# Optimization experiments

Measured on AMD Instinct MI355X. Metric: run time of the kernel, lower is better.

The kernel has to match this reference:

```python
import jax, jax.numpy as jnp
import numpy as np

D_MODEL = 512
NHEAD = 8
DK = D_MODEL // NHEAD
DIM_FF = 2048
LN_EPS = 1e-5


def setup_inputs() -> dict:
    key = jax.random.key(0)
    ks = jax.random.split(key, 12)
    B, L = 8, 1024
    s = 1.0 / np.sqrt(D_MODEL)
    sf = 1.0 / np.sqrt(DIM_FF)
    return {
        "x": jax.random.normal(ks[0], (B, L, D_MODEL), jnp.float32),
        "key_padding_mask": jnp.zeros((B, L), dtype=bool),
        "bias": jax.random.normal(ks[1], (B, L, L), jnp.float32),
        # projection weights stored [in, out] so y = x @ W + b (matches torch Linear math)
        "Wq": jax.random.normal(ks[2], (D_MODEL, D_MODEL), jnp.float32) * s,
        "bq": jnp.zeros((D_MODEL,), jnp.float32),
        "Wk": jax.random.normal(ks[3], (D_MODEL, D_MODEL), jnp.float32) * s,
        "bk": jnp.zeros((D_MODEL,), jnp.float32),
        "Wv": jax.random.normal(ks[4], (D_MODEL, D_MODEL), jnp.float32) * s,
        "bv": jnp.zeros((D_MODEL,), jnp.float32),
        "Wo": jax.random.normal(ks[5], (D_MODEL, D_MODEL), jnp.float32) * s,
        "bo": jnp.zeros((D_MODEL,), jnp.float32),
        "ln1_g": jnp.ones((D_MODEL,), jnp.float32),
        "ln1_b": jnp.zeros((D_MODEL,), jnp.float32),
        "W1": jax.random.normal(ks[6], (D_MODEL, DIM_FF), jnp.float32) * s,
        "b1": jnp.zeros((DIM_FF,), jnp.float32),
        "W2": jax.random.normal(ks[7], (DIM_FF, D_MODEL), jnp.float32) * sf,
        "b2": jnp.zeros((D_MODEL,), jnp.float32),
        "ln2_g": jnp.ones((D_MODEL,), jnp.float32),
        "ln2_b": jnp.zeros((D_MODEL,), jnp.float32),
    }


def _layernorm(x, g, b):
    mu = jnp.mean(x, axis=-1, keepdims=True)
    var = jnp.mean(jnp.square(x - mu), axis=-1, keepdims=True)
    return (x - mu) * jax.lax.rsqrt(var + LN_EPS) * g + b


def reference(x, key_padding_mask, bias, Wq, bq, Wk, bk, Wv, bv, Wo, bo,
              ln1_g, ln1_b, W1, b1, W2, b2, ln2_g, ln2_b):
    B, L, H = x.shape
    residual = x
    # [B, L, D] -> [B, nhead, L, dk]
    q = (x @ Wq + bq).reshape(B, L, NHEAD, DK).transpose(0, 2, 1, 3)
    k = (x @ Wk + bk).reshape(B, L, NHEAD, DK).transpose(0, 2, 1, 3)
    v = (x @ Wv + bv).reshape(B, L, NHEAD, DK).transpose(0, 2, 1, 3)
    scores = jnp.einsum("bhqd,bhkd->bhqk", q, k) / np.sqrt(DK)
    scores = scores + bias[:, None, :, :]
    scores = jnp.where(key_padding_mask[:, None, None, :], -jnp.inf, scores)
    attn = jax.nn.softmax(scores, axis=-1)  # dropout p=0 (eval)
    out = jnp.einsum("bhqk,bhkd->bhqd", attn, v)
    out = out.transpose(0, 2, 1, 3).reshape(B, L, H)
    out = out @ Wo + bo
    x = _layernorm(residual + out, ln1_g, ln1_b)
    residual = x
    h = jax.nn.relu(x @ W1 + b1)
    x = h @ W2 + b2
    return _layernorm(residual + x, ln2_g, ln2_b)
```

## Files before the change

### kernel.cpp

```cpp
#include <hip/hip_runtime.h>
#include <math.h>

#define NHEAD 8
#define DKD 64
#define DMODEL 512
#define LSEQ 1024
#define NBL 8192

typedef __attribute__((ext_vector_type(8))) short bf8;
typedef __attribute__((ext_vector_type(4))) float f4;

__device__ inline unsigned short f2bf(float f) {
    union { float f; unsigned u; } v; v.f = f;
    unsigned r = v.u + 0x7FFFu + ((v.u >> 16) & 1u);
    return (unsigned short)(r >> 16);
}

__device__ __forceinline__ unsigned cvtpk(float lo, float hi) {
    unsigned r;
    asm("v_cvt_pk_bf16_f32 %0, %1, %2" : "=v"(r) : "v"(lo), "v"(hi));
    return r;
}

__device__ __forceinline__ void gload16(const void* g, void* l) {
    __builtin_amdgcn_global_load_lds(
        (const __attribute__((address_space(1))) unsigned int*)g,
        (__attribute__((address_space(3))) unsigned int*)l, 16, 0, 0);
}

__global__ __launch_bounds__(256) void conv_bf16(
    const float* __restrict__ in, unsigned short* __restrict__ out, int n)
{
    int i = (blockIdx.x * 256 + threadIdx.x) * 4;
    if (i >= n) return;
    float4 v = *(const float4*)(in + i);
    ushort4 o;
    o.x = f2bf(v.x); o.y = f2bf(v.y); o.z = f2bf(v.z); o.w = f2bf(v.w);
    *(ushort4*)(out + i) = o;
}

__global__ __launch_bounds__(256) void biasm_kernel(
    const float* __restrict__ bias, const unsigned char* __restrict__ mask,
    float* __restrict__ o)
{
    int i = blockIdx.x * 256 + threadIdx.x;
    int flat = i * 4;
    int b = flat >> 20;
    int k = flat & 1023;
    float4 v = ((const float4*)bias)[i];
    uchar4 mk = *(const uchar4*)(mask + b * 1024 + k);
    if (mk.x) v.x = -1e30f;
    if (mk.y) v.y = -1e30f;
    if (mk.z) v.z = -1e30f;
    if (mk.w) v.w = -1e30f;
    ((float4*)o)[i] = v;
}

__device__ __forceinline__ void do_transpose(
    const float* __restrict__ W, unsigned short* __restrict__ Wt,
    int K, int N, int bx, int by)
{
    __shared__ float tile[64][65];
    const int k0 = by * 64, n0 = bx * 64;
    const int c = threadIdx.x & 63, r0 = (threadIdx.x >> 6) * 16;
    #pragma unroll
    for (int i = 0; i < 16; ++i)
        tile[r0 + i][c] = W[(size_t)(k0 + r0 + i) * N + n0 + c];
    __syncthreads();
    #pragma unroll
    for (int i = 0; i < 16; ++i)
        Wt[(size_t)(n0 + r0 + i) * K + k0 + c] = f2bf(tile[c][r0 + i]);
}

__global__ __launch_bounds__(256) void prep_weights(
    const float* __restrict__ Wq, const float* __restrict__ Wk,
    const float* __restrict__ Wv, const float* __restrict__ Wo,
    const float* __restrict__ W1, const float* __restrict__ W2,
    const float* __restrict__ bq, const float* __restrict__ bk,
    const float* __restrict__ bv,
    unsigned short* __restrict__ Wqkv, unsigned short* __restrict__ Wot,
    unsigned short* __restrict__ W1t, unsigned short* __restrict__ W2t,
    float* __restrict__ bqkv)
{
    int j = blockIdx.x;
    if (j < 256) {
        int which = j >> 6, tt = j & 63;
        const float* src = which == 0 ? Wq : which == 1 ? Wk : which == 2 ? Wv : Wo;
        unsigned short* dst = which == 0 ? Wqkv : which == 1 ? (Wqkv + 262144)
                            : which == 2 ? (Wqkv + 524288) : Wot;
        do_transpose(src, dst, 512, 512, tt & 7, tt >> 3);
    } else if (j < 512) {
        int tt = j - 256;
        do_transpose(W1, W1t, 512, 2048, tt & 31, tt >> 5);
    } else if (j < 768) {
        int tt = j - 512;
        do_transpose(W2, W2t, 2048, 512, tt & 7, tt >> 3);
    } else {
        for (int c = threadIdx.x; c < 1536; c += 256)
            bqkv[c] = c < 512 ? bq[c] : c < 1024 ? bk[c - 512] : bv[c - 1024];
    }
}

template<int BN>
__global__ __launch_bounds__(256) void mfma_gemm(
    const unsigned short* __restrict__ A, const unsigned short* __restrict__ Bt,
    const float* __restrict__ bias, const float* __restrict__ resid,
    void* __restrict__ outp, int M, int N, int K, int relu, int outmode,
    unsigned short* __restrict__ qs, unsigned short* __restrict__ ks,
    unsigned short* __restrict__ vts)
{
    __shared__ uint4 As[1024];
    __shared__ uint4 Bs[BN * 8];
    constexpr int NB = BN / 32;

    const int t = threadIdx.x;
    const int lane = t & 63, w = t >> 6;
    const int g = lane >> 4, r15 = lane & 15;
    const int wr = w >> 1, wc = w & 1;
    const int rowBase = blockIdx.y * 128, colBase = blockIdx.x * BN;

    f4 acc[4][NB] = {};

    const int r   = t >> 3;
    const int chs = (t & 7) ^ (r & 7);
    unsigned short* Al = (unsigned short*)As + (w * 8) * 64;
    unsigned short* Bl = (unsigned short*)Bs + (w * 8) * 64;

    for (int k0 = 0; k0 < K; k0 += 64) {
        __syncthreads();
        {
            const unsigned short* Ag = A  + (size_t)(rowBase + r) * K + k0 + chs * 8;
            const unsigned short* Bg = Bt + (size_t)(colBase + r) * K + k0 + chs * 8;
            #pragma unroll
            for (int p = 0; p < 4; ++p)
                gload16(Ag + (size_t)(p * 32) * K, Al + p * 32 * 64);
            #pragma unroll
            for (int p = 0; p < BN / 32; ++p)
                gload16(Bg + (size_t)(p * 32) * K, Bl + p * 32 * 64);
        }
        __syncthreads();
        #pragma unroll
        for (int kk = 0; kk < 2; ++kk) {
            bf8 af[4], bfr[NB];
            #pragma unroll
            for (int m = 0; m < 4; ++m) {
                int ra = wr * 64 + m * 16 + r15;
                af[m] = *(const bf8*)&As[ra * 8 + ((kk * 4 + g) ^ (ra & 7))];
            }
            #pragma unroll
            for (int n = 0; n < NB; ++n) {
                int rb = wc * (BN / 2) + n * 16 + r15;
                bfr[n] = *(const bf8*)&Bs[rb * 8 + ((kk * 4 + g) ^ (rb & 7))];
            }
            #pragma unroll
            for (int m = 0; m < 4; ++m)
                #pragma unroll
                for (int n = 0; n < NB; ++n)
                    acc[m][n] = __builtin_amdgcn_mfma_f32_16x16x32_bf16(
                        af[m], bfr[n], acc[m][n], 0, 0, 0);
        }
    }

    #pragma unroll
    for (int m = 0; m < 4; ++m) {
        #pragma unroll
        for (int n = 0; n < NB; ++n) {
            int col = colBase + wc * (BN / 2) + n * 16 + r15;
            float bv = bias[col];
            #pragma unroll
            for (int rr = 0; rr < 4; ++rr) {
                int row = rowBase + wr * 64 + m * 16 + g * 4 + rr;
                float v = acc[m][n][rr] + bv;
                if (relu) v = fmaxf(v, 0.f);
                if (outmode == 0) {
                    size_t idx = (size_t)row * N + col;
                    if (resid) v += resid[idx];
                    ((float*)outp)[idx] = v;
                } else if (outmode == 1) {
                    ((unsigned short*)outp)[(size_t)row * N + col] = f2bf(v);
                } else {
                    int sel = col >> 9, hd = col & 511;
                    int h = hd >> 6, dk = hd & 63;
                    int b = row >> 10, l = row & 1023;
                    unsigned short bw = f2bf(v);
                    size_t bh = (size_t)(b * NHEAD + h);
                    if (sel == 0)      qs[(bh * LSEQ + l) * DKD + dk] = bw;
                    else if (sel == 1) ks[(bh * LSEQ + l) * DKD + dk] = bw;
                    else               vts[(bh * DKD + dk) * LSEQ + l] = bw;
                }
            }
        }
    }
}

__global__ __launch_bounds__(256) void attn_mfma(
    const unsigned short* __restrict__ Qg, const unsigned short* __restrict__ Kg,
    const unsigned short* __restrict__ Vtg, const float* __restrict__ biasM,
    unsigned short* __restrict__ Ob)
{
    __shared__ uint4 Ks[2][512];
    __shared__ uint4 Vs[2][512];
    __shared__ unsigned int Pb[4096];

    const int t = threadIdx.x;
    const int lane = t & 63, w = t >> 6;
    const int g = lane >> 4, r15 = lane & 15;

    const int p = blockIdx.x;
    const int logical = (p & 7) * 64 + (p >> 3);
    const int bh = logical >> 3, qt = logical & 7;
    const int b = bh >> 3, h = bh & 7;
    const int qbase = qt * 128 + w * 32;

    bf8 qf[2][2];
    #pragma unroll
    for (int u = 0; u < 2; ++u) {
        const unsigned short* qp = Qg + ((size_t)bh * LSEQ + qbase + u * 16 + r15) * DKD + g * 8;
        qf[u][0] = *(const bf8*)qp;
        qf[u][1] = *(const bf8*)(qp + 32);
    }

    float mrun[2] = {-1e30f, -1e30f}, lsum[2] = {0.f, 0.f};
    f4 oacc[2][4] = {};

    const int sr  = t >> 3;
    const int chs = (t & 7) ^ (sr & 7);
    unsigned int* Pw = Pb + w * 1024;

    const size_t kBase = (size_t)bh * LSEQ * DKD;
    const size_t vBase = (size_t)bh * DKD * LSEQ;

    {
        const unsigned short* Kgp = Kg  + kBase + (size_t)sr * DKD + chs * 8;
        const unsigned short* Vgp = Vtg + vBase + (size_t)sr * LSEQ + chs * 8;
        unsigned short* Kl = (unsigned short*)Ks[0] + (w * 8) * 64;
        unsigned short* Vl = (unsigned short*)Vs[0] + (w * 8) * 64;
        gload16(Kgp, Kl);
        gload16(Kgp + (size_t)32 * DKD, Kl + 32 * 64);
        gload16(Vgp, Vl);
        gload16(Vgp + (size_t)32 * LSEQ, Vl + 32 * 64);
    }
    __syncthreads();

    for (int kt = 0; kt < 16; ++kt) {
        const int cur = kt & 1;
        const int key0 = kt * 64;
        if (kt < 15) {
            const int nk0 = key0 + 64;
            const unsigned short* Kgp = Kg  + kBase + (size_t)(nk0 + sr) * DKD + chs * 8;
            const unsigned short* Vgp = Vtg + vBase + (size_t)sr * LSEQ + nk0 + chs * 8;
            unsigned short* Kl = (unsigned short*)Ks[cur ^ 1] + (w * 8) * 64;
            unsigned short* Vl = (unsigned short*)Vs[cur ^ 1] + (w * 8) * 64;
            gload16(Kgp, Kl);
            gload16(Kgp + (size_t)32 * DKD, Kl + 32 * 64);
            gload16(Vgp, Vl);
            gload16(Vgp + (size_t)32 * LSEQ, Vl + 32 * 64);
        }

        f4 sacc[2][4] = {};
        #pragma unroll
        for (int kk = 0; kk < 2; ++kk)
            #pragma unroll
            for (int m = 0; m < 4; ++m) {
                int row = m * 16 + r15;
                bf8 kf = *(const bf8*)&Ks[cur][row * 8 + ((kk * 4 + g) ^ (row & 7))];
                sacc[0][m] = __builtin_amdgcn_mfma_f32_16x16x32_bf16(kf, qf[0][kk], sacc[0][m], 0, 0, 0);
                sacc[1][m] = __builtin_amdgcn_mfma_f32_16x16x32_bf16(kf, qf[1][kk], sacc[1][m], 0, 0, 0);
            }

        #pragma unroll
        for (int u = 0; u < 2; ++u) {
            const float* biasRow = biasM + ((size_t)b << 20)
                                 + (size_t)(qbase + u * 16 + r15) * LSEQ + key0;
            float s[16];
            float pmax = -1e30f;
            #pragma unroll
            for (int m = 0; m < 4; ++m) {
                float4 bv = *(const float4*)(biasRow + m * 16 + g * 4);
                const float* bvp = (const float*)&bv;
                #pragma unroll
                for (int j = 0; j < 4; ++j) {
                    float sv = fmaf(sacc[u][m][j], 0.125f, bvp[j]);
                    s[m * 4 + j] = sv;
                    pmax = fmaxf(pmax, sv);
                }
            }
            pmax = fmaxf(pmax, __shfl_xor(pmax, 16));
            pmax = fmaxf(pmax, __shfl_xor(pmax, 32));

            if (!__all(pmax <= mrun[u] + 8.f)) {
                float mnew = fmaxf(mrun[u], pmax);
                float scale = __expf(mrun[u] - mnew);
                lsum[u] *= scale;
                #pragma unroll
                for (int m = 0; m < 4; ++m)
                    #pragma unroll
                    for (int j = 0; j < 4; ++j) oacc[u][m][j] *= scale;
                mrun[u] = mnew;
            }

            float psum = 0.f;
            #pragma unroll
            for (int i = 0; i < 16; ++i) { s[i] = __expf(s[i] - mrun[u]); psum += s[i]; }
            psum += __shfl_xor(psum, 16);
            psum += __shfl_xor(psum, 32);
            lsum[u] += psum;

            #pragma unroll
            for (int m = 0; m < 4; ++m) {
                uint2 pk;
                pk.x = cvtpk(s[m * 4 + 0], s[m * 4 + 1]);
                pk.y = cvtpk(s[m * 4 + 2], s[m * 4 + 3]);
                int off = ((u * 16 + r15) * 128 + m * 32 + g * 8) ^ ((r15 & 7) << 4);
                *(uint2*)((char*)Pw + off) = pk;
            }
        }

        #pragma unroll
        for (int kk = 0; kk < 2; ++kk) {
            bf8 pf[2];
            #pragma unroll
            for (int u = 0; u < 2; ++u) {
                int off = ((u * 16 + r15) * 128 + kk * 64 + g * 16) ^ ((r15 & 7) << 4);
                pf[u] = *(const bf8*)((char*)Pw + off);
            }
            #pragma unroll
            for (int m = 0; m < 4; ++m) {
                int row = m * 16 + r15;
                bf8 vf = *(const bf8*)&Vs[cur][row * 8 + ((kk * 4 + g) ^ (row & 7))];
                oacc[0][m] = __builtin_amdgcn_mfma_f32_16x16x32_bf16(vf, pf[0], oacc[0][m], 0, 0, 0);
                oacc[1][m] = __builtin_amdgcn_mfma_f32_16x16x32_bf16(vf, pf[1], oacc[1][m], 0, 0, 0);
            }
        }
        __syncthreads();
    }

    #pragma unroll
    for (int u = 0; u < 2; ++u) {
        float inv = 1.f / lsum[u];
        unsigned short* op = Ob + ((size_t)b * LSEQ + qbase + u * 16 + r15) * DMODEL + h * DKD;
        #pragma unroll
        for (int m = 0; m < 4; ++m) {
            ushort4 o4;
            o4.x = f2bf(oacc[u][m][0] * inv);
            o4.y = f2bf(oacc[u][m][1] * inv);
            o4.z = f2bf(oacc[u][m][2] * inv);
            o4.w = f2bf(oacc[u][m][3] * inv);
            *(ushort4*)(op + m * 16 + g * 4) = o4;
        }
    }
}

__global__ __launch_bounds__(256) void ln_kernel(
    const float* __restrict__ in, const float* __restrict__ g,
    const float* __restrict__ bt, float* __restrict__ out,
    unsigned short* __restrict__ outb)
{
    const int row  = blockIdx.x * 4 + (threadIdx.x >> 6);
    const int lane = threadIdx.x & 63;
    const float* rp = in + (size_t)row * DMODEL + lane * 8;
    float4 x0 = *(const float4*)rp;
    float4 x1 = *(const float4*)(rp + 4);
    float xs[8] = {x0.x, x0.y, x0.z, x0.w, x1.x, x1.y, x1.z, x1.w};

    float sum = 0.f;
    #pragma unroll
    for (int i = 0; i < 8; ++i) sum += xs[i];
    #pragma unroll
    for (int off = 32; off; off >>= 1) sum += __shfl_xor(sum, off);
    float mu = sum * (1.f / 512.f);

    float vs = 0.f;
    #pragma unroll
    for (int i = 0; i < 8; ++i) { float d = xs[i] - mu; vs += d * d; }
    #pragma unroll
    for (int off = 32; off; off >>= 1) vs += __shfl_xor(vs, off);
    float rs = rsqrtf(vs * (1.f / 512.f) + 1e-5f);

    const float* gp = g  + lane * 8;
    const float* bp = bt + lane * 8;
    float4 g0 = *(const float4*)gp, g1 = *(const float4*)(gp + 4);
    float4 b0 = *(const float4*)bp, b1 = *(const float4*)(bp + 4);
    float gs[8] = {g0.x, g0.y, g0.z, g0.w, g1.x, g1.y, g1.z, g1.w};
    float bs[8] = {b0.x, b0.y, b0.z, b0.w, b1.x, b1.y, b1.z, b1.w};

    float res[8];
    #pragma unroll
    for (int i = 0; i < 8; ++i) res[i] = (xs[i] - mu) * rs * gs[i] + bs[i];

    float* op = out + (size_t)row * DMODEL + lane * 8;
    float4 r0 = {res[0], res[1], res[2], res[3]};
    float4 r1 = {res[4], res[5], res[6], res[7]};
    *(float4*)op       = r0;
    *(float4*)(op + 4) = r1;

    if (outb) {
        unsigned short* ob = outb + (size_t)row * DMODEL + lane * 8;
        ushort4 u0, u1;
        u0.x = f2bf(res[0]); u0.y = f2bf(res[1]); u0.z = f2bf(res[2]); u0.w = f2bf(res[3]);
        u1.x = f2bf(res[4]); u1.y = f2bf(res[5]); u1.z = f2bf(res[6]); u1.w = f2bf(res[7]);
        *(ushort4*)ob       = u0;
        *(ushort4*)(ob + 4) = u1;
    }
}

extern "C" void kernel_launch(void* const* d_in, const int* in_sizes, int n_in,
                              void* d_out, int out_size, void* d_ws, size_t ws_size,
                              hipStream_t stream)
{
    const float*         x    = (const float*)d_in[0];
    const unsigned char* mask = (const unsigned char*)d_in[1];
    const float*         bias = (const float*)d_in[2];
    const float* Wq = (const float*)d_in[3];
    const float* bq = (const float*)d_in[4];
    const float* Wk = (const float*)d_in[5];
    const float* bk = (const float*)d_in[6];
    const float* Wv = (const float*)d_in[7];
    const float* bv = (const float*)d_in[8];
    const float* Wo = (const float*)d_in[9];
    const float* bo = (const float*)d_in[10];
    const float* ln1g = (const float*)d_in[11];
    const float* ln1b = (const float*)d_in[12];
    const float* W1 = (const float*)d_in[13];
    const float* b1 = (const float*)d_in[14];
    const float* W2 = (const float*)d_in[15];
    const float* b2 = (const float*)d_in[16];
    const float* ln2g = (const float*)d_in[17];
    const float* ln2b = (const float*)d_in[18];

    char* W = (char*)d_ws;
    unsigned short* Qb   = (unsigned short*)(W);
    unsigned short* Kb   = (unsigned short*)(W + (8u << 20));
    unsigned short* Vtb  = (unsigned short*)(W + (16u << 20));
    unsigned short* Oball= (unsigned short*)(W + (24u << 20));
    unsigned short* hb   = (unsigned short*)(W);
    float*          biasM= (float*)(W + (32u << 20));
    float*          y12  = (float*)(W + (32u << 20));
    float*          x1   = (float*)(W + (48u << 20));
    unsigned short* xb   = (unsigned short*)(W + (66u << 20));
    unsigned short* x1b  = xb;
    unsigned short* Wqkv = (unsigned short*)(W + (74u << 20));
    unsigned short* Wot  = (unsigned short*)(W + (76u << 20));
    unsigned short* W1t  = (unsigned short*)(W + (77u << 20));
    unsigned short* W2t  = (unsigned short*)(W + (79u << 20));
    float*          bqkv = (float*)(W + (81u << 20));
    float*          outp = (float*)d_out;

    conv_bf16<<<dim3(4096), dim3(256), 0, stream>>>(x, xb, NBL * DMODEL);
    prep_weights<<<dim3(769), dim3(256), 0, stream>>>(
        Wq, Wk, Wv, Wo, W1, W2, bq, bk, bv, Wqkv, Wot, W1t, W2t, bqkv);
    biasm_kernel<<<dim3(8192), dim3(256), 0, stream>>>(bias, mask, biasM);

    mfma_gemm<128><<<dim3(12, 64), dim3(256), 0, stream>>>(
        xb, Wqkv, bqkv, nullptr, nullptr, NBL, 1536, 512, 0, 2, Qb, Kb, Vtb);

    attn_mfma<<<dim3(512), dim3(256), 0, stream>>>(Qb, Kb, Vtb, biasM, Oball);

    mfma_gemm<64><<<dim3(8, 64), dim3(256), 0, stream>>>(
        Oball, Wot, bo, x, y12, NBL, 512, 512, 0, 0, nullptr, nullptr, nullptr);

    ln_kernel<<<dim3(NBL / 4), dim3(256), 0, stream>>>(y12, ln1g, ln1b, x1, x1b);

    mfma_gemm<128><<<dim3(16, 64), dim3(256), 0, stream>>>(
        x1b, W1t, b1, nullptr, hb, NBL, 2048, 512, 1, 1, nullptr, nullptr, nullptr);

    mfma_gemm<64><<<dim3(8, 64), dim3(256), 0, stream>>>(
        hb, W2t, b2, x1, y12, NBL, 512, 2048, 0, 0, nullptr, nullptr, nullptr);

    ln_kernel<<<dim3(NBL / 4), dim3(256), 0, stream>>>(y12, ln2g, ln2b, outp, nullptr);
}
```

Baseline: 358.4 us.

## Fuse mask into attention, double-buffer GEMM LDS, prefetch bias tiles

Removes the separate bias+mask kernel and applies the key padding mask inside the attention kernel, which reads the raw bias directly. This avoids writing and re-reading a 32 MB masked bias buffer. The attention loop is unrolled by two and prefetches the bias and mask for the next tile into registers while the current tile computes, and it raises wave priority around the MFMA blocks. The GEMM gets double-buffered LDS so the next K slice loads while the current one computes, at the cost of twice the shared memory and possibly lower occupancy.

```diff
diff --git a/kernel.cpp b/kernel.cpp
--- a/kernel.cpp
+++ b/kernel.cpp
@@ -37,23 +37,6 @@
     ushort4 o;
     o.x = f2bf(v.x); o.y = f2bf(v.y); o.z = f2bf(v.z); o.w = f2bf(v.w);
     *(ushort4*)(out + i) = o;
-}
-
-__global__ __launch_bounds__(256) void biasm_kernel(
-    const float* __restrict__ bias, const unsigned char* __restrict__ mask,
-    float* __restrict__ o)
-{
-    int i = blockIdx.x * 256 + threadIdx.x;
-    int flat = i * 4;
-    int b = flat >> 20;
-    int k = flat & 1023;
-    float4 v = ((const float4*)bias)[i];
-    uchar4 mk = *(const uchar4*)(mask + b * 1024 + k);
-    if (mk.x) v.x = -1e30f;
-    if (mk.y) v.y = -1e30f;
-    if (mk.z) v.z = -1e30f;
-    if (mk.w) v.w = -1e30f;
-    ((float4*)o)[i] = v;
 }
 
 __device__ __forceinline__ void do_transpose(
@@ -109,8 +92,8 @@
     unsigned short* __restrict__ qs, unsigned short* __restrict__ ks,
     unsigned short* __restrict__ vts)
 {
-    __shared__ uint4 As[1024];
-    __shared__ uint4 Bs[BN * 8];
+    __shared__ uint4 As[2][1024];
+    __shared__ uint4 Bs[2][BN * 8];
     constexpr int NB = BN / 32;
 
     const int t = threadIdx.x;
@@ -123,34 +106,41 @@
 
     const int r   = t >> 3;
     const int chs = (t & 7) ^ (r & 7);
-    unsigned short* Al = (unsigned short*)As + (w * 8) * 64;
-    unsigned short* Bl = (unsigned short*)Bs + (w * 8) * 64;
-
-    for (int k0 = 0; k0 < K; k0 += 64) {
-        __syncthreads();
-        {
-            const unsigned short* Ag = A  + (size_t)(rowBase + r) * K + k0 + chs * 8;
-            const unsigned short* Bg = Bt + (size_t)(colBase + r) * K + k0 + chs * 8;
-            #pragma unroll
-            for (int p = 0; p < 4; ++p)
-                gload16(Ag + (size_t)(p * 32) * K, Al + p * 32 * 64);
-            #pragma unroll
-            for (int p = 0; p < BN / 32; ++p)
-                gload16(Bg + (size_t)(p * 32) * K, Bl + p * 32 * 64);
-        }
-        __syncthreads();
+    const unsigned short* Ag0 = A  + (size_t)(rowBase + r) * K + chs * 8;
+    const unsigned short* Bg0 = Bt + (size_t)(colBase + r) * K + chs * 8;
+
+    auto stage = [&](int buf, int k0) {
+        unsigned short* Al = (unsigned short*)As[buf] + (w * 8) * 64;
+        unsigned short* Bl = (unsigned short*)Bs[buf] + (w * 8) * 64;
+        const unsigned short* Ag = Ag0 + k0;
+        const unsigned short* Bg = Bg0 + k0;
+        #pragma unroll
+        for (int p = 0; p < 4; ++p)
+            gload16(Ag + (size_t)(p * 32) * K, Al + p * 32 * 64);
+        #pragma unroll
+        for (int p = 0; p < NB; ++p)
+            gload16(Bg + (size_t)(p * 32) * K, Bl + p * 32 * 64);
+    };
+
+    const int nst = K >> 6;
+    stage(0, 0);
+    __syncthreads();
+
+    for (int it = 0; it < nst; ++it) {
+        const int cur = it & 1;
+        if (it + 1 < nst) stage(cur ^ 1, (it + 1) << 6);
         #pragma unroll
         for (int kk = 0; kk < 2; ++kk) {
             bf8 af[4], bfr[NB];
             #pragma unroll
             for (int m = 0; m < 4; ++m) {
                 int ra = wr * 64 + m * 16 + r15;
-                af[m] = *(const bf8*)&As[ra * 8 + ((kk * 4 + g) ^ (ra & 7))];
+                af[m] = *(const bf8*)&As[cur][ra * 8 + ((kk * 4 + g) ^ (ra & 7))];
             }
             #pragma unroll
             for (int n = 0; n < NB; ++n) {
                 int rb = wc * (BN / 2) + n * 16 + r15;
-                bfr[n] = *(const bf8*)&Bs[rb * 8 + ((kk * 4 + g) ^ (rb & 7))];
+                bfr[n] = *(const bf8*)&Bs[cur][rb * 8 + ((kk * 4 + g) ^ (rb & 7))];
             }
             #pragma unroll
             for (int m = 0; m < 4; ++m)
@@ -159,6 +149,7 @@
                     acc[m][n] = __builtin_amdgcn_mfma_f32_16x16x32_bf16(
                         af[m], bfr[n], acc[m][n], 0, 0, 0);
         }
+        __syncthreads();
     }
 
     #pragma unroll
@@ -193,10 +184,117 @@
     }
 }
 
+struct TileRegs { float4 b[2][4]; unsigned mk[4]; };
+
+__device__ __forceinline__ void load_tile_regs(
+    TileRegs& tr, const float* bR0, const float* bR1,
+    const unsigned char* mrow, int key0, int g)
+{
+    #pragma unroll
+    for (int m = 0; m < 4; ++m) {
+        tr.b[0][m] = *(const float4*)(bR0 + key0 + m * 16 + g * 4);
+        tr.b[1][m] = *(const float4*)(bR1 + key0 + m * 16 + g * 4);
+        tr.mk[m]   = *(const unsigned*)(mrow + key0 + m * 16 + g * 4);
+    }
+}
+
+__device__ __forceinline__ void attn_tile(
+    const uint4* __restrict__ Kb, const uint4* __restrict__ Vb,
+    const TileRegs& tr, bf8 (&qf)[2][2], f4 (&oacc)[2][4],
+    float (&mrun)[2], float (&lsum)[2],
+    unsigned short* Pw, int g, int r15)
+{
+    f4 sacc[2][4] = {};
+    __builtin_amdgcn_s_setprio(1);
+    #pragma unroll
+    for (int kk = 0; kk < 2; ++kk)
+        #pragma unroll
+        for (int m = 0; m < 4; ++m) {
+            int row = m * 16 + r15;
+            bf8 kf = *(const bf8*)&Kb[row * 8 + ((kk * 4 + g) ^ (row & 7))];
+            sacc[0][m] = __builtin_amdgcn_mfma_f32_16x16x32_bf16(kf, qf[0][kk], sacc[0][m], 0, 0, 0);
+            sacc[1][m] = __builtin_amdgcn_mfma_f32_16x16x32_bf16(kf, qf[1][kk], sacc[1][m], 0, 0, 0);
+        }
+    __builtin_amdgcn_s_setprio(0);
+
+    float madd[16];
+    #pragma unroll
+    for (int m = 0; m < 4; ++m) {
+        unsigned mku = tr.mk[m];
+        #pragma unroll
+        for (int j = 0; j < 4; ++j)
+            madd[m * 4 + j] = ((mku >> (8 * j)) & 0xffu) ? -1e30f : 0.f;
+    }
+
+    #pragma unroll
+    for (int u = 0; u < 2; ++u) {
+        float s[16];
+        float pmax = -1e30f;
+        #pragma unroll
+        for (int m = 0; m < 4; ++m) {
+            const float* bvp = (const float*)&tr.b[u][m];
+            #pragma unroll
+            for (int j = 0; j < 4; ++j) {
+                float sv = fmaf(sacc[u][m][j], 0.125f, bvp[j] + madd[m * 4 + j]);
+                s[m * 4 + j] = sv;
+                pmax = fmaxf(pmax, sv);
+            }
+        }
+        pmax = fmaxf(pmax, __shfl_xor(pmax, 16));
+        pmax = fmaxf(pmax, __shfl_xor(pmax, 32));
+
+        if (!__all(pmax <= mrun[u] + 8.f)) {
+            float mnew = fmaxf(mrun[u], pmax);
+            float scale = __expf(mrun[u] - mnew);
+            lsum[u] *= scale;
+            #pragma unroll
+            for (int m = 0; m < 4; ++m)
+                #pragma unroll
+                for (int j = 0; j < 4; ++j) oacc[u][m][j] *= scale;
+            mrun[u] = mnew;
+        }
+
+        float psum = 0.f;
+        #pragma unroll
+        for (int i = 0; i < 16; ++i) { s[i] = __expf(s[i] - mrun[u]); psum += s[i]; }
+        psum += __shfl_xor(psum, 16);
+        psum += __shfl_xor(psum, 32);
+        lsum[u] += psum;
+
+        #pragma unroll
+        for (int m = 0; m < 4; ++m) {
+            uint2 pk;
+            pk.x = cvtpk(s[m * 4 + 0], s[m * 4 + 1]);
+            pk.y = cvtpk(s[m * 4 + 2], s[m * 4 + 3]);
+            int off = ((u * 16 + r15) * 128 + m * 32 + g * 8) ^ ((r15 & 7) << 4);
+            *(uint2*)((char*)Pw + off) = pk;
+        }
+    }
+
+    #pragma unroll
+    for (int kk = 0; kk < 2; ++kk) {
+        bf8 pf[2];
+        #pragma unroll
+        for (int u = 0; u < 2; ++u) {
+            int off = ((u * 16 + r15) * 128 + kk * 64 + g * 16) ^ ((r15 & 7) << 4);
+            pf[u] = *(const bf8*)((char*)Pw + off);
+        }
+        __builtin_amdgcn_s_setprio(1);
+        #pragma unroll
+        for (int m = 0; m < 4; ++m) {
+            int row = m * 16 + r15;
+            bf8 vf = *(const bf8*)&Vb[row * 8 + ((kk * 4 + g) ^ (row & 7))];
+            oacc[0][m] = __builtin_amdgcn_mfma_f32_16x16x32_bf16(vf, pf[0], oacc[0][m], 0, 0, 0);
+            oacc[1][m] = __builtin_amdgcn_mfma_f32_16x16x32_bf16(vf, pf[1], oacc[1][m], 0, 0, 0);
+        }
+        __builtin_amdgcn_s_setprio(0);
+    }
+}
+
 __global__ __launch_bounds__(256) void attn_mfma(
     const unsigned short* __restrict__ Qg, const unsigned short* __restrict__ Kg,
-    const unsigned short* __restrict__ Vtg, const float* __restrict__ biasM,
-    unsigned short* __restrict__ Ob)
+    const unsigned short* __restrict__ Vtg, const float* __restrict__ bias,
+    const unsigned char* __restrict__ mask, unsigned short* __restrict__ Ob)
 {
     __shared__ uint4 Ks[2][512];
     __shared__ uint4 Vs[2][512];
@@ -225,113 +323,42 @@
 
     const int sr  = t >> 3;
     const int chs = (t & 7) ^ (sr & 7);
-    unsigned int* Pw = Pb + w * 1024;
+    unsigned short* Pw = (unsigned short*)(Pb + w * 1024);
 
     const size_t kBase = (size_t)bh * LSEQ * DKD;
     const size_t vBase = (size_t)bh * DKD * LSEQ;
 
-    {
-        const unsigned short* Kgp = Kg  + kBase + (size_t)sr * DKD + chs * 8;
-        const unsigned short* Vgp = Vtg + vBase + (size_t)sr * LSEQ + chs * 8;
-        unsigned short* Kl = (unsigned short*)Ks[0] + (w * 8) * 64;
-        unsigned short* Vl = (unsigned short*)Vs[0] + (w * 8) * 64;
+    const float* bR0 = bias + ((size_t)b << 20) + (size_t)(qbase + r15) * LSEQ;
+    const float* bR1 = bias + ((size_t)b << 20) + (size_t)(qbase + 16 + r15) * LSEQ;
+    const unsigned char* mrow = mask + b * LSEQ;
+
+    auto stage = [&](uint4* Kbuf, uint4* Vbuf, int key0) {
+        const unsigned short* Kgp = Kg  + kBase + (size_t)(key0 + sr) * DKD + chs * 8;
+        const unsigned short* Vgp = Vtg + vBase + (size_t)sr * LSEQ + key0 + chs * 8;
+        unsigned short* Kl = (unsigned short*)Kbuf + (w * 8) * 64;
+        unsigned short* Vl = (unsigned short*)Vbuf + (w * 8) * 64;
         gload16(Kgp, Kl);
         gload16(Kgp + (size_t)32 * DKD, Kl + 32 * 64);
         gload16(Vgp, Vl);
         gload16(Vgp + (size_t)32 * LSEQ, Vl + 32 * 64);
-    }
+    };
+
+    TileRegs trA, trB;
+    load_tile_regs(trA, bR0, bR1, mrow, 0, g);
+    stage(Ks[0], Vs[0], 0);
     __syncthreads();
 
-    for (int kt = 0; kt < 16; ++kt) {
-        const int cur = kt & 1;
-        const int key0 = kt * 64;
-        if (kt < 15) {
-            const int nk0 = key0 + 64;
-            const unsigned short* Kgp = Kg  + kBase + (size_t)(nk0 + sr) * DKD + chs * 8;
-            const unsigned short* Vgp = Vtg + vBase + (size_t)sr * LSEQ + nk0 + chs * 8;
-            unsigned short* Kl = (unsigned short*)Ks[cur ^ 1] + (w * 8) * 64;
-            unsigned short* Vl = (unsigned short*)Vs[cur ^ 1] + (w * 8) * 64;
-            gload16(Kgp, Kl);
-            gload16(Kgp + (size_t)32 * DKD, Kl + 32 * 64);
-            gload16(Vgp, Vl);
-            gload16(Vgp + (size_t)32 * LSEQ, Vl + 32 * 64);
-        }
-
-        f4 sacc[2][4] = {};
-        #pragma unroll
-        for (int kk = 0; kk < 2; ++kk)
-            #pragma unroll
-            for (int m = 0; m < 4; ++m) {
-                int row = m * 16 + r15;
-                bf8 kf = *(const bf8*)&Ks[cur][row * 8 + ((kk * 4 + g) ^ (row & 7))];
-                sacc[0][m] = __builtin_amdgcn_mfma_f32_16x16x32_bf16(kf, qf[0][kk], sacc[0][m], 0, 0, 0);
-                sacc[1][m] = __builtin_amdgcn_mfma_f32_16x16x32_bf16(kf, qf[1][kk], sacc[1][m], 0, 0, 0);
-            }
-
-        #pragma unroll
-        for (int u = 0; u < 2; ++u) {
-            const float* biasRow = biasM + ((size_t)b << 20)
-                                 + (size_t)(qbase + u * 16 + r15) * LSEQ + key0;
-            float s[16];
-            float pmax = -1e30f;
-            #pragma unroll
-            for (int m = 0; m < 4; ++m) {
-                float4 bv = *(const float4*)(biasRow + m * 16 + g * 4);
-                const float* bvp = (const float*)&bv;
-                #pragma unroll
-                for (int j = 0; j < 4; ++j) {
-                    float sv = fmaf(sacc[u][m][j], 0.125f, bvp[j]);
-                    s[m * 4 + j] = sv;
-                    pmax = fmaxf(pmax, sv);
-                }
-            }
-            pmax = fmaxf(pmax, __shfl_xor(pmax, 16));
-            pmax = fmaxf(pmax, __shfl_xor(pmax, 32));
-
-            if (!__all(pmax <= mrun[u] + 8.f)) {
-                float mnew = fmaxf(mrun[u], pmax);
-                float scale = __expf(mrun[u] - mnew);
-                lsum[u] *= scale;
-                #pragma unroll
-                for (int m = 0; m < 4; ++m)
-                    #pragma unroll
-                    for (int j = 0; j < 4; ++j) oacc[u][m][j] *= scale;
-                mrun[u] = mnew;
-            }
-
-            float psum = 0.f;
-            #pragma unroll
-            for (int i = 0; i < 16; ++i) { s[i] = __expf(s[i] - mrun[u]); psum += s[i]; }
-            psum += __shfl_xor(psum, 16);
-            psum += __shfl_xor(psum, 32);
-            lsum[u] += psum;
-
-            #pragma unroll
-            for (int m = 0; m < 4; ++m) {
-                uint2 pk;
-                pk.x = cvtpk(s[m * 4 + 0], s[m * 4 + 1]);
-                pk.y = cvtpk(s[m * 4 + 2], s[m * 4 + 3]);
-                int off = ((u * 16 + r15) * 128 + m * 32 + g * 8) ^ ((r15 & 7) << 4);
-                *(uint2*)((char*)Pw + off) = pk;
-            }
-        }
-
-        #pragma unroll
-        for (int kk = 0; kk < 2; ++kk) {
-            bf8 pf[2];
-            #pragma unroll
-            for (int u = 0; u < 2; ++u) {
-                int off = ((u * 16 + r15) * 128 + kk * 64 + g * 16) ^ ((r15 & 7) << 4);
-                pf[u] = *(const bf8*)((char*)Pw + off);
-            }
-            #pragma unroll
-            for (int m = 0; m < 4; ++m) {
-                int row = m * 16 + r15;
-                bf8 vf = *(const bf8*)&Vs[cur][row * 8 + ((kk * 4 + g) ^ (row & 7))];
-                oacc[0][m] = __builtin_amdgcn_mfma_f32_16x16x32_bf16(vf, pf[0], oacc[0][m], 0, 0, 0);
-                oacc[1][m] = __builtin_amdgcn_mfma_f32_16x16x32_bf16(vf, pf[1], oacc[1][m], 0, 0, 0);
-            }
-        }
+    for (int kt2 = 0; kt2 < 8; ++kt2) {
+        const int keyE = kt2 * 128;
+        stage(Ks[1], Vs[1], keyE + 64);
+        load_tile_regs(trB, bR0, bR1, mrow, keyE + 64, g);
+        attn_tile(Ks[0], Vs[0], trA, qf, oacc, mrun, lsum, Pw, g, r15);
+        __syncthreads();
+        if (kt2 < 7) {
+            stage(Ks[0], Vs[0], keyE + 128);
+            load_tile_regs(trA, bR0, bR1, mrow, keyE + 128, g);
+        }
+        attn_tile(Ks[1], Vs[1], trB, qf, oacc, mrun, lsum, Pw, g, r15);
         __syncthreads();
     }
 
@@ -434,7 +461,6 @@
     unsigned short* Vtb  = (unsigned short*)(W + (16u << 20));
     unsigned short* Oball= (unsigned short*)(W + (24u << 20));
     unsigned short* hb   = (unsigned short*)(W);
-    float*          biasM= (float*)(W + (32u << 20));
     float*          y12  = (float*)(W + (32u << 20));
     float*          x1   = (float*)(W + (48u << 20));
     unsigned short* xb   = (unsigned short*)(W + (66u << 20));
@@ -449,12 +475,11 @@
     conv_bf16<<<dim3(4096), dim3(256), 0, stream>>>(x, xb, NBL * DMODEL);
     prep_weights<<<dim3(769), dim3(256), 0, stream>>>(
         Wq, Wk, Wv, Wo, W1, W2, bq, bk, bv, Wqkv, Wot, W1t, W2t, bqkv);
-    biasm_kernel<<<dim3(8192), dim3(256), 0, stream>>>(bias, mask, biasM);
 
     mfma_gemm<128><<<dim3(12, 64), dim3(256), 0, stream>>>(
         xb, Wqkv, bqkv, nullptr, nullptr, NBL, 1536, 512, 0, 2, Qb, Kb, Vtb);
 
-    attn_mfma<<<dim3(512), dim3(256), 0, stream>>>(Qb, Kb, Vtb, biasM, Oball);
+    attn_mfma<<<dim3(512), dim3(256), 0, stream>>>(Qb, Kb, Vtb, bias, mask, Oball);
 
     mfma_gemm<64><<<dim3(8, 64), dim3(256), 0, stream>>>(
         Oball, Wot, bo, x, y12, NBL, 512, 512, 0, 0, nullptr, nullptr, nullptr);
```

New measurement: 383.1 us. +6.9%, slower.
